# Optimization experiments

Hardware: AMD Instinct MI355X
Metric: run time of the kernel (lower is better)

Reference implementation:

```python
import jax, jax.numpy as jnp
from jax import lax
import numpy as np

NUM_HEAD = 4
D_MODEL = 160
HEAD_DIM = D_MODEL // NUM_HEAD  # 40
FEAT_DIM = 64
F_SIZE = (128, 128)
B = 4
LN_EPS = 1e-5
LEAKY_SLOPE = 0.01
DN = ('NCHW', 'OIHW', 'NCHW')


def setup_inputs() -> dict:
    key = jax.random.key(0)
    ks = jax.random.split(key, 10)
    pe_len = (F_SIZE[0] // 2) * (F_SIZE[1] // 2) + 1  # 4097
    s = 0.05
    return {
        'x': jax.random.normal(ks[0], (B, FEAT_DIM, F_SIZE[0], F_SIZE[1]), jnp.float32),
        'conv1_w': jax.random.normal(ks[1], (FEAT_DIM, FEAT_DIM, 2, 2), jnp.float32) * s,
        'conv1_b': jax.random.normal(ks[2], (FEAT_DIM,), jnp.float32) * s,
        'conv2_w': jax.random.normal(ks[3], (D_MODEL, FEAT_DIM, 1, 1), jnp.float32) * s,
        'conv2_b': jax.random.normal(ks[4], (D_MODEL,), jnp.float32) * s,
        'pe': jax.random.uniform(ks[5], (pe_len, 1), jnp.float32),
        'wq': jax.random.normal(ks[6], (D_MODEL, D_MODEL), jnp.float32) * s,
        'wk': jax.random.normal(ks[7], (D_MODEL, D_MODEL), jnp.float32) * s,
        'wv': jax.random.normal(ks[8], (D_MODEL, D_MODEL), jnp.float32) * s,
        'ln_w': jnp.ones((D_MODEL,), jnp.float32),
        'ln_b': jnp.zeros((D_MODEL,), jnp.float32),
    }


def reference(x, conv1_w, conv1_b, conv2_w, conv2_b, pe, wq, wk, wv, ln_w, ln_b):
    b = x.shape[0]
    # patch embed: stride-2 conv -> 1x1 conv -> LeakyReLU
    f = lax.conv_general_dilated(x, conv1_w, (2, 2), 'VALID', dimension_numbers=DN)
    f = f + conv1_b[None, :, None, None]
    f = lax.conv_general_dilated(f, conv2_w, (1, 1), 'VALID', dimension_numbers=DN)
    f = f + conv2_b[None, :, None, None]
    f = jnp.where(f >= 0, f, LEAKY_SLOPE * f)
    _, c, h, w = f.shape  # [b, 160, 64, 64]
    f = f.reshape(b, c, h * w).transpose(0, 2, 1)  # [b, s, d]
    # pad one extra token at end of sequence, add positional encoding [s+1, 1]
    f = jnp.pad(f, ((0, 0), (0, 1), (0, 0))) + pe  # [b, s+1, d]
    s1 = f.shape[1]
    # torch Linear (no bias): y = x @ W.T
    q = (f @ wq.T).reshape(b, s1, NUM_HEAD, HEAD_DIM).transpose(0, 2, 1, 3)
    k = (f @ wk.T).reshape(b, s1, NUM_HEAD, HEAD_DIM).transpose(0, 2, 1, 3)
    v = (f @ wv.T).reshape(b, s1, NUM_HEAD, HEAD_DIM).transpose(0, 2, 1, 3)
    score = jnp.einsum('bhqd,bhkd->bhqk', q, k) / jnp.sqrt(jnp.float32(HEAD_DIM))
    score = jax.nn.softmax(score, axis=-1)
    att = jnp.einsum('bhqk,bhkd->bhqd', score, v)  # [b, h, s+1, hd]
    cat = att.transpose(0, 2, 1, 3).reshape(b, s1, D_MODEL)
    feat = cat[:, :-1, :]  # drop padded token -> [b, s, d]
    # residual LayerNorm: LN(feat) + feat
    mu = jnp.mean(feat, axis=-1, keepdims=True)
    var = jnp.mean(jnp.square(feat - mu), axis=-1, keepdims=True)
    ln = (feat - mu) / jnp.sqrt(var + LN_EPS) * ln_w + ln_b
    feat = ln + feat
    feat = feat.transpose(0, 2, 1).reshape(b, D_MODEL, h, w)  # [b, 160, 64, 64]
    feat = jnp.repeat(jnp.repeat(feat, 2, axis=2), 2, axis=3)
    return feat
```

## Files before the change

### kernel.cpp

```cpp
#include <hip/hip_runtime.h>

typedef _Float16 f16;
typedef _Float16 half2v __attribute__((ext_vector_type(2)));
typedef _Float16 half4v __attribute__((ext_vector_type(4)));
typedef _Float16 half8 __attribute__((ext_vector_type(8)));
typedef float f32x4 __attribute__((ext_vector_type(4)));
typedef unsigned u32x4 __attribute__((ext_vector_type(4)));

#define MFMA16(a, b, c) __builtin_amdgcn_mfma_f32_16x16x32_f16((a), (b), (c), 0, 0, 0)

__device__ __forceinline__ unsigned pk2(float a, float b) {
  return __builtin_bit_cast(unsigned, __builtin_amdgcn_cvt_pkrtz(a, b));
}

__device__ __forceinline__ void plswap_pair(unsigned& a, unsigned& b) {
  asm("s_nop 1\n\t"
      "v_permlane32_swap_b32 %0, %1\n\t"
      "v_permlane16_swap_b32 %0, %1"
      : "+v"(a), "+v"(b));
}


__global__ __launch_bounds__(256) void k_convqkv(
    const float* __restrict__ x, const float* __restrict__ w1, const float* __restrict__ b1,
    const float* __restrict__ w2, const float* __restrict__ b2, const float* __restrict__ pe,
    const float* __restrict__ wq, const float* __restrict__ wk, const float* __restrict__ wv,
    f16* __restrict__ q_h, f16* __restrict__ k_h, f16* __restrict__ vt_h,
    float* __restrict__ kmaxp) {
  __shared__ __attribute__((aligned(16))) char smem[112192];
  f16* fT   = (f16*)smem;
  f16* xh   = (f16*)(smem + 21504);
  f16* wT   = (f16*)(smem + 21504);
  float* red = (float*)(smem + 48384);
  f16* w1h  = (f16*)(smem + 55360);
  f16* c1t  = (f16*)(smem + 55360);
  f16* Lv   = (f16*)(smem + 55360);
  float* red160 = (float*)(smem + 64576);
  f16* w2h  = (f16*)(smem + 89152);

  const float c1l = 0.15811388300841898f * 1.4426950408889634f;

  int y = blockIdx.x, b = blockIdx.y;
  int t = threadIdx.x, lane = t & 63, wv4 = t >> 6, quad = lane >> 4, col = lane & 15;
  int s0 = y * 64;

  const float* xb = x + (b * 64) * 16384 + (2 * y) * 128;
#pragma unroll
  for (int it = 0; it < 32; ++it) {
    int flat = t + it * 256;
    int pos = flat & 63, r = (flat >> 6) & 1, ci = flat >> 7;
    float2 v = *(const float2*)(xb + ci * 16384 + r * 128 + 2 * pos);
    *(unsigned*)(xh + pos * 264 + ci * 4 + r * 2) = pk2(v.x, v.y);
  }
#pragma unroll
  for (int it = 0; it < 16; ++it) {
    int i4 = t + it * 256;
    int co = i4 >> 6, q4 = (i4 & 63) * 4;
    f32x4 v = *(const f32x4*)(w1 + co * 256 + q4);
    uint2 u = {pk2(v[0], v[1]), pk2(v[2], v[3])};
    *(uint2*)(w1h + co * 264 + q4) = u;
  }
#pragma unroll
  for (int it = 0; it < 10; ++it) {
    int i4 = t + it * 256;
    int c2 = i4 >> 4, q4 = (i4 & 15) * 4;
    f32x4 v = *(const f32x4*)(w2 + c2 * 64 + q4);
    uint2 u = {pk2(v[0], v[1]), pk2(v[2], v[3])};
    *(uint2*)(w2h + c2 * 72 + q4) = u;
  }
  __syncthreads();

  float b1v[4];
#pragma unroll
  for (int r = 0; r < 4; ++r) b1v[r] = b1[wv4 * 16 + quad * 4 + r];
  f32x4 acc1[4];
#pragma unroll
  for (int nt = 0; nt < 4; ++nt)
#pragma unroll
    for (int r = 0; r < 4; ++r) acc1[nt][r] = b1v[r];
#pragma unroll
  for (int kk = 0; kk < 8; ++kk) {
    half8 a = *(half8*)(w1h + (wv4 * 16 + col) * 264 + kk * 32 + quad * 8);
#pragma unroll
    for (int nt = 0; nt < 4; ++nt) {
      half8 bfr = *(half8*)(xh + (nt * 16 + col) * 264 + kk * 32 + quad * 8);
      acc1[nt] = MFMA16(a, bfr, acc1[nt]);
    }
  }
  __syncthreads();
#pragma unroll
  for (int nt = 0; nt < 4; ++nt) {
    uint2 u = {pk2(acc1[nt][0], acc1[nt][1]), pk2(acc1[nt][2], acc1[nt][3])};
    *(uint2*)(c1t + (nt * 16 + col) * 72 + wv4 * 16 + quad * 4) = u;
  }
  __syncthreads();

  f32x4 acc2[10];
#pragma unroll
  for (int mt = 0; mt < 10; ++mt)
#pragma unroll
    for (int r = 0; r < 4; ++r) acc2[mt][r] = b2[mt * 16 + quad * 4 + r];
  half8 bb0 = *(half8*)(c1t + (wv4 * 16 + col) * 72 + quad * 8);
  half8 bb1 = *(half8*)(c1t + (wv4 * 16 + col) * 72 + 32 + quad * 8);
#pragma unroll
  for (int mt = 0; mt < 10; ++mt) {
    half8 a0 = *(half8*)(w2h + (mt * 16 + col) * 72 + quad * 8);
    half8 a1 = *(half8*)(w2h + (mt * 16 + col) * 72 + 32 + quad * 8);
    acc2[mt] = MFMA16(a0, bb0, acc2[mt]);
    acc2[mt] = MFMA16(a1, bb1, acc2[mt]);
  }
  float pes = pe[s0 + wv4 * 16 + col];
#pragma unroll
  for (int mt = 0; mt < 10; ++mt) {
    float p[4];
#pragma unroll
    for (int r = 0; r < 4; ++r) {
      float v = acc2[mt][r];
      v = (v >= 0.f) ? v : 0.01f * v;
      p[r] = v + pes;
    }
    uint2 u = {pk2(p[0], p[1]), pk2(p[2], p[3])};
    *(uint2*)(fT + (wv4 * 16 + col) * 168 + mt * 16 + quad * 4) = u;
  }
  __syncthreads();

  half8 af[5];
  int rowA = wv4 * 16 + col;
#pragma unroll
  for (int kk = 0; kk < 5; ++kk)
    af[kk] = *(half8*)(fT + rowA * 168 + kk * 32 + quad * 8);

  float ks0[4], ks1[4];
#pragma unroll
  for (int r = 0; r < 4; ++r) { ks0[r] = 0.f; ks1[r] = 0.f; }

  for (int kind = 0; kind < 3; ++kind) {
    const float* wsp = (kind == 0) ? wq : (kind == 1 ? wk : wv);
    for (int hf = 0; hf < 2; ++hf) {
      __syncthreads();
      for (int c = t; c < 1600; c += 256) {
        int row = c / 20, seg = c - row * 20;
        const float* src = wsp + (hf * 80 + row) * 160 + seg * 8;
        f32x4 va = *(const f32x4*)src;
        f32x4 vb = *(const f32x4*)(src + 4);
        uint4 u = {pk2(va[0], va[1]), pk2(va[2], va[3]), pk2(vb[0], vb[1]), pk2(vb[2], vb[3])};
        *(uint4*)(wT + row * 168 + seg * 8) = u;
      }
      __syncthreads();
#pragma unroll
      for (int n0 = 0; n0 < 5; ++n0) {
        f32x4 acc; acc[0] = 0.f; acc[1] = 0.f; acc[2] = 0.f; acc[3] = 0.f;
        int rowB = n0 * 16 + col;
#pragma unroll
        for (int kk = 0; kk < 5; ++kk) {
          half8 bf = *(half8*)(wT + rowB * 168 + kk * 32 + quad * 8);
          acc = MFMA16(af[kk], bf, acc);
        }
        int o = (hf * 5 + n0) * 16 + col;
        int hh = o / 40, d = o - hh * 40;
        int bh = b * 4 + hh;
        if (kind == 1) {
          bool kidx = (n0 * 16 + col) >= 40;
#pragma unroll
          for (int r = 0; r < 4; ++r) {
            float z = acc[r] * acc[r];
            ks0[r] += kidx ? 0.f : z;
            ks1[r] += kidx ? z : 0.f;
          }
        }
        if (kind == 2) {
          half4v hv;
#pragma unroll
          for (int r = 0; r < 4; ++r) hv[r] = (f16)acc[r];
          *(half4v*)(Lv + (n0 * 16 + col) * 72 + wv4 * 16 + quad * 4) = hv;
        } else {
#pragma unroll
          for (int r = 0; r < 4; ++r) {
            int s = s0 + wv4 * 16 + quad * 4 + r;
            if (kind == 0)      q_h[((size_t)bh * 4097 + s) * 40 + d] = (f16)(acc[r] * c1l);
            else                k_h[((size_t)bh * 4160 + s) * 40 + d] = (f16)acc[r];
          }
        }
      }
      if (kind == 1) {
        float m0 = 0.f, m1 = 0.f;
#pragma unroll
        for (int r = 0; r < 4; ++r) {
          float v0 = ks0[r], v1 = ks1[r];
          v0 += __shfl_xor(v0, 1); v0 += __shfl_xor(v0, 2);
          v0 += __shfl_xor(v0, 4); v0 += __shfl_xor(v0, 8);
          v1 += __shfl_xor(v1, 1); v1 += __shfl_xor(v1, 2);
          v1 += __shfl_xor(v1, 4); v1 += __shfl_xor(v1, 8);
          m0 = fmaxf(m0, v0); m1 = fmaxf(m1, v1);
          ks0[r] = 0.f; ks1[r] = 0.f;
        }
        m0 = fmaxf(m0, __shfl_xor(m0, 16)); m0 = fmaxf(m0, __shfl_xor(m0, 32));
        m1 = fmaxf(m1, __shfl_xor(m1, 16)); m1 = fmaxf(m1, __shfl_xor(m1, 32));
        if (lane == 0) { red[wv4 * 4 + hf * 2] = m0; red[wv4 * 4 + hf * 2 + 1] = m1; }
      }
      if (kind == 2) {
        __syncthreads();
        for (int c = t; c < 640; c += 256) {
          int row = c >> 3, seg = c & 7;
          int o = hf * 80 + row, hh = o / 40, d = o - hh * 40;
          *(uint4*)(vt_h + ((size_t)(b * 4 + hh) * 40 + d) * 4160 + s0 + seg * 8) =
              *(const uint4*)(Lv + row * 72 + seg * 8);
        }
      }
    }
  }
  __syncthreads();
  if (t < 4) {
    float m = fmaxf(fmaxf(red[t], red[4 + t]), fmaxf(red[8 + t], red[12 + t]));
    kmaxp[(b * 4 + t) * 65 + y] = m;
  }

  if (y == 63) {
    float pe4 = pe[4096];
    if (t < 160) {
      int hh = t / 40, d = t - hh * 40, bh = b * 4 + hh;
#pragma unroll
      for (int kind = 0; kind < 3; ++kind) {
        const float* wsp = (kind == 0) ? wq : (kind == 1 ? wk : wv);
        const float* wr = wsp + t * 160;
        float rs = 0.f;
#pragma unroll
        for (int c4 = 0; c4 < 40; ++c4) {
          f32x4 v = *(const f32x4*)(wr + c4 * 4);
          rs += v[0] + v[1] + v[2] + v[3];
        }
        float val = pe4 * rs;
        if (kind == 0)      q_h[((size_t)bh * 4097 + 4096) * 40 + d] = (f16)(val * c1l);
        else if (kind == 1) { k_h[((size_t)bh * 4160 + 4096) * 40 + d] = (f16)val;
                              red160[t] = val * val; }
        else                vt_h[((size_t)bh * 40 + d) * 4160 + 4096] = (f16)val;
      }
    }
    __syncthreads();
    if (t < 4) {
      float s = 0.f;
#pragma unroll
      for (int j = 0; j < 40; ++j) s += red160[t * 40 + j];
      kmaxp[(b * 4 + t) * 65 + 64] = s;
    }
  }
}

__global__ __launch_bounds__(256, 6) void k_attn(
    const f16* __restrict__ q_h, const f16* __restrict__ k_h,
    const f16* __restrict__ vt_h, const float* __restrict__ kmaxp,
    float* __restrict__ pacc) {
  __shared__ __attribute__((aligned(16))) f16 Ks[2][64 * 40];
  __shared__ __attribute__((aligned(16))) f16 Vs[2][40 * 72];
  __shared__ __attribute__((aligned(16))) f16 Ones[8];
  __shared__ __attribute__((aligned(16))) f16 Zro[8];
  __shared__ __attribute__((aligned(16))) float red4[4];

  int qt = blockIdx.x, bh = blockIdx.y, ks = blockIdx.z;
  int qbase = qt * 128;
  int t = threadIdx.x, lane = t & 63, wv = t >> 6, quad = lane >> 4, col = lane & 15;
  int gbase = ks * 22;
  int nIter = (ks == 2) ? 21 : 22;

  if (t < 8) { Zro[t] = (f16)0; Ones[t] = (f16)1; }
  {
    float vm = (t < 65) ? kmaxp[bh * 65 + t] : 0.f;
#pragma unroll
    for (int d = 1; d < 64; d <<= 1) vm = fmaxf(vm, __shfl_xor(vm, d));
    if (lane == 0) red4[wv] = vm;
  }

  const f16* khb = k_h + ((size_t)bh * 4160 + gbase * 64) * 40;
  const f16* vtb = vt_h + (size_t)bh * 40 * 4160;
  int vrow = t >> 3, vseg = t & 7;
  uint4 rka = *(const uint4*)(khb + t * 8);
  uint4 rkb = {0, 0, 0, 0}, rvb = {0, 0, 0, 0};
  if (t < 64) rkb = *(const uint4*)(khb + (256 + t) * 8);
  uint4 rva = *(const uint4*)(vtb + vrow * 4160 + gbase * 64 + vseg * 8);
  if (t < 64) rvb = *(const uint4*)(vtb + (32 + vrow) * 4160 + gbase * 64 + vseg * 8);

  half8 zero8;
#pragma unroll
  for (int j = 0; j < 8; ++j) zero8[j] = (f16)0;

  half8 bq[2][2], q32[2];
#pragma unroll
  for (int nt = 0; nt < 2; ++nt) {
    const f16* qr = q_h + ((size_t)bh * 4097 + qbase + wv * 32 + nt * 16 + col) * 40;
    bq[nt][0] = *(const half8*)(qr + quad * 8);
    q32[nt] = *(const half8*)(qr + 32);
  }
  __syncthreads();

  float mk = fmaxf(fmaxf(red4[0], red4[1]), fmaxf(red4[2], red4[3]));

#pragma unroll
  for (int nt = 0; nt < 2; ++nt) {
    float s = 0.f;
#pragma unroll
    for (int j = 0; j < 8; ++j) {
      float a0 = (float)bq[nt][0][j];
      s += a0 * a0;
    }
    s += __shfl_xor(s, 16);
    s += __shfl_xor(s, 32);
#pragma unroll
    for (int j = 0; j < 8; ++j) {
      float a1 = (float)q32[nt][j];
      s += a1 * a1;
    }
    float mfl = sqrtf(s * mk) - 14.0f;
    half8 e = zero8;
    e[0] = (f16)(-mfl);
    bq[nt][1] = (quad == 0) ? q32[nt] : ((quad == 1) ? e : zero8);
  }

  f32x4 o_[2][3];
#pragma unroll
  for (int a = 0; a < 2; ++a)
#pragma unroll
    for (int b2 = 0; b2 < 3; ++b2)
#pragma unroll
      for (int r = 0; r < 4; ++r) o_[a][b2][r] = 0.f;

  for (int kt = 0; kt < nIter; ++kt) {
    int bsel = kt & 1;
    int g = gbase + kt;
    *(uint4*)(&Ks[bsel][t * 8]) = rka;
    if (t < 64) *(uint4*)(&Ks[bsel][(256 + t) * 8]) = rkb;
    *(uint4*)(&Vs[bsel][vrow * 72 + vseg * 8]) = rva;
    if (t < 64) *(uint4*)(&Vs[bsel][(32 + vrow) * 72 + vseg * 8]) = rvb;
    if (kt + 1 < nIter) {
      const f16* kn = khb + (size_t)(kt + 1) * 2560;
      int k0n = (g + 1) << 6;
      rka = *(const uint4*)(kn + t * 8);
      if (t < 64) rkb = *(const uint4*)(kn + (256 + t) * 8);
      rva = *(const uint4*)(vtb + vrow * 4160 + k0n + vseg * 8);
      if (t < 64) rvb = *(const uint4*)(vtb + (32 + vrow) * 4160 + k0n + vseg * 8);
    }
    __syncthreads();

    bool lastt = (g == 64);
#pragma unroll
    for (int kk2 = 0; kk2 < 2; ++kk2) {
      f32x4 acc[2][2];
#pragma unroll
      for (int hf = 0; hf < 2; ++hf) {
        int mt = kk2 * 2 + hf;
        int row = mt * 16 + col;
        half8 ak0 = *(half8*)(&Ks[bsel][row * 40 + quad * 8]);
        const f16* pa1 = (quad == 0) ? &Ks[bsel][row * 40 + 32]
                                     : ((quad == 1) ? Ones : Zro);
        half8 ak1 = *(half8*)pa1;
#pragma unroll
        for (int nt = 0; nt < 2; ++nt) {
          f32x4 a; a[0] = 0.f; a[1] = 0.f; a[2] = 0.f; a[3] = 0.f;
          a = MFMA16(ak0, bq[nt][0], a);
          a = MFMA16(ak1, bq[nt][1], a);
          acc[hf][nt] = a;
        }
      }
      half8 pa[2];
#pragma unroll
      for (int nt = 0; nt < 2; ++nt) {
        float p0[4], p1[4];
#pragma unroll
        for (int r = 0; r < 4; ++r) {
          p0[r] = __builtin_amdgcn_exp2f(acc[0][nt][r]);
          p1[r] = __builtin_amdgcn_exp2f(acc[1][nt][r]);
        }
        if (__builtin_expect(lastt, 0)) {
#pragma unroll
          for (int r = 0; r < 4; ++r) {
            p0[r] = ((kk2 * 2) * 16 + quad * 4 + r) == 0 ? p0[r] : 0.f;
            p1[r] = 0.f;
          }
        }
        unsigned sr[4];
        sr[0] = pk2(p0[0], p0[1]);
        sr[1] = pk2(p0[2], p0[3]);
        sr[2] = pk2(p1[0], p1[1]);
        sr[3] = pk2(p1[2], p1[3]);
        plswap_pair(sr[0], sr[2]);
        plswap_pair(sr[1], sr[3]);
        u32x4 uu; uu[0] = sr[0]; uu[1] = sr[1]; uu[2] = sr[2]; uu[3] = sr[3];
        pa[nt] = __builtin_bit_cast(half8, uu);
      }
#pragma unroll
      for (int nv = 0; nv < 3; ++nv) {
        int d = nv * 16 + col;
        const f16* vp = (d < 40) ? &Vs[bsel][d * 72 + kk2 * 32 + quad * 8]
                                 : ((d == 40) ? Ones : Zro);
        half8 bv = *(half8*)vp;
        o_[0][nv] = MFMA16(pa[0], bv, o_[0][nv]);
        o_[1][nv] = MFMA16(pa[1], bv, o_[1][nv]);
      }
    }
  }

  float* pb = pacc + (size_t)(ks * 16 + bh) * 4096 * 48;
#pragma unroll
  for (int mtq = 0; mtq < 2; ++mtq)
#pragma unroll
    for (int nv = 0; nv < 3; ++nv)
#pragma unroll
      for (int r = 0; r < 4; ++r) {
        int q = qbase + wv * 32 + mtq * 16 + quad * 4 + r;
        pb[(size_t)q * 48 + nv * 16 + col] = o_[mtq][nv][r];
      }
}

__global__ __launch_bounds__(256) void k_ln_out(
    const float* __restrict__ pacc, const float* __restrict__ lnw,
    const float* __restrict__ lnb, float* __restrict__ out) {
  __shared__ float g[32 * 164];
  __shared__ float linv[32 * 4];
  int y = blockIdx.x, b = blockIdx.y, z = blockIdx.z, t = threadIdx.x;
  const size_t P1 = (size_t)16 * 4096 * 48;
  int w0 = z * 32;
  if (t < 128) {
    int row = t >> 2, h = t & 3;
    size_t i0 = ((size_t)(b * 4 + h) * 4096 + y * 64 + w0 + row) * 48 + 40;
    linv[row * 4 + h] = 1.f / (pacc[i0] + pacc[P1 + i0] + pacc[2 * P1 + i0]);
  }
  __syncthreads();
#pragma unroll
  for (int it = 0; it < 5; ++it) {
    int flat = t + it * 256;
    int row = flat / 40, dq = flat - row * 40;
    int h = dq / 10, d = (dq - h * 10) * 4;
    size_t idx = ((size_t)(b * 4 + h) * 4096 + y * 64 + w0 + row) * 48 + d;
    f32x4 v0 = *(const f32x4*)(pacc + idx);
    f32x4 v1 = *(const f32x4*)(pacc + P1 + idx);
    f32x4 v2 = *(const f32x4*)(pacc + 2 * P1 + idx);
    float li = linv[row * 4 + h];
    f32x4 gv;
#pragma unroll
    for (int j = 0; j < 4; ++j) gv[j] = (v0[j] + v1[j] + v2[j]) * li;
    *(f32x4*)(g + row * 164 + h * 40 + d) = gv;
  }
  __syncthreads();
  int row = t >> 3, part = t & 7;
  float* gr = g + row * 164 + part * 20;
  float s1 = 0.f, s2 = 0.f;
#pragma unroll
  for (int j4 = 0; j4 < 5; ++j4) {
    f32x4 v = *(f32x4*)(gr + j4 * 4);
#pragma unroll
    for (int j = 0; j < 4; ++j) { s1 += v[j]; s2 += v[j] * v[j]; }
  }
  s1 += __shfl_xor(s1, 1); s1 += __shfl_xor(s1, 2); s1 += __shfl_xor(s1, 4);
  s2 += __shfl_xor(s2, 1); s2 += __shfl_xor(s2, 2); s2 += __shfl_xor(s2, 4);
  float mu = s1 * (1.f / 160.f);
  float var = s2 * (1.f / 160.f) - mu * mu;
  float inv = rsqrtf(var + 1e-5f);
  const float* lw = lnw + part * 20;
  const float* lb = lnb + part * 20;
#pragma unroll
  for (int j = 0; j < 20; ++j) {
    float v = gr[j];
    gr[j] = (v - mu) * inv * lw[j] + lb[j] + v;
  }
  __syncthreads();
  int Yo = t >> 7, xp = t & 63, cpar = (t >> 6) & 1;
  int rl = xp >> 1;
  float* ob = out + (2 * y + Yo) * 128 + z * 64 + xp;
  for (int c = cpar; c < 160; c += 2)
    ob[(size_t)(b * 160 + c) * 16384] = g[rl * 164 + c];
}

extern "C" void kernel_launch(void* const* d_in, const int* in_sizes, int n_in,
                              void* d_out, int out_size, void* d_ws, size_t ws_size,
                              hipStream_t stream) {
  const float* x   = (const float*)d_in[0];
  const float* w1  = (const float*)d_in[1];
  const float* b1  = (const float*)d_in[2];
  const float* w2  = (const float*)d_in[3];
  const float* b2  = (const float*)d_in[4];
  const float* pe  = (const float*)d_in[5];
  const float* wq  = (const float*)d_in[6];
  const float* wk  = (const float*)d_in[7];
  const float* wvp = (const float*)d_in[8];
  const float* lnw = (const float*)d_in[9];
  const float* lnb = (const float*)d_in[10];
  float* out = (float*)d_out;

  char* p = (char*)d_ws;
  f16* q_h   = (f16*)p;   p += (size_t)16 * 4097 * 40 * 2;
  f16* k_h   = (f16*)p;   p += (size_t)16 * 4160 * 40 * 2;
  f16* vt_h  = (f16*)p;   p += (size_t)16 * 40 * 4160 * 2;
  float* pacc = (float*)p; p += (size_t)3 * 16 * 4096 * 48 * 4;
  float* kmaxp = (float*)p; p += 16 * 65 * 4;

  k_convqkv<<<dim3(64, 4), 256, 0, stream>>>(x, w1, b1, w2, b2, pe, wq, wk, wvp,
                                             q_h, k_h, vt_h, kmaxp);
  k_attn<<<dim3(32, 16, 3), 256, 0, stream>>>(q_h, k_h, vt_h, kmaxp, pacc);
  k_ln_out<<<dim3(64, 4, 2), 256, 0, stream>>>(pacc, lnw, lnb, out);
}
```

Before: 245.9 us.

## Split attention keys into two chunks and batch QK MFMAs per tile

The key-sequence split in the attention kernel drops from three partitions to two (33 and 32 tiles). The partial-accumulator buffer and the LayerNorm combine step shrink to match, so one partial buffer is no longer written and read. Each 64-key tile now computes all four QK score blocks before the exp and PV stage, which gives more independent MFMAs per tile but uses more registers, so the occupancy hint drops from 6 to 4 blocks. This cuts partial-result traffic, but the grid falls to 1024 blocks and per-block serial work grows.

```diff
diff --git a/kernel.cpp b/kernel.cpp
--- a/kernel.cpp
+++ b/kernel.cpp
@@ -246,7 +246,7 @@
   }
 }
 
-__global__ __launch_bounds__(256, 6) void k_attn(
+__global__ __launch_bounds__(256, 4) void k_attn(
     const f16* __restrict__ q_h, const f16* __restrict__ k_h,
     const f16* __restrict__ vt_h, const float* __restrict__ kmaxp,
     float* __restrict__ pacc) {
@@ -259,8 +259,8 @@
   int qt = blockIdx.x, bh = blockIdx.y, ks = blockIdx.z;
   int qbase = qt * 128;
   int t = threadIdx.x, lane = t & 63, wv = t >> 6, quad = lane >> 4, col = lane & 15;
-  int gbase = ks * 22;
-  int nIter = (ks == 2) ? 21 : 22;
+  int gbase = ks * 33;
+  int nIter = 33 - ks;
 
   if (t < 8) { Zro[t] = (f16)0; Ones[t] = (f16)1; }
   {
@@ -341,38 +341,39 @@
     __syncthreads();
 
     bool lastt = (g == 64);
-#pragma unroll
-    for (int kk2 = 0; kk2 < 2; ++kk2) {
-      f32x4 acc[2][2];
-#pragma unroll
-      for (int hf = 0; hf < 2; ++hf) {
-        int mt = kk2 * 2 + hf;
-        int row = mt * 16 + col;
-        half8 ak0 = *(half8*)(&Ks[bsel][row * 40 + quad * 8]);
-        const f16* pa1 = (quad == 0) ? &Ks[bsel][row * 40 + 32]
-                                     : ((quad == 1) ? Ones : Zro);
-        half8 ak1 = *(half8*)pa1;
-#pragma unroll
-        for (int nt = 0; nt < 2; ++nt) {
-          f32x4 a; a[0] = 0.f; a[1] = 0.f; a[2] = 0.f; a[3] = 0.f;
-          a = MFMA16(ak0, bq[nt][0], a);
-          a = MFMA16(ak1, bq[nt][1], a);
-          acc[hf][nt] = a;
-        }
-      }
-      half8 pa[2];
+
+    f32x4 acc[4][2];
+#pragma unroll
+    for (int mt = 0; mt < 4; ++mt) {
+      int row = mt * 16 + col;
+      half8 ak0 = *(half8*)(&Ks[bsel][row * 40 + quad * 8]);
+      const f16* pa1 = (quad == 0) ? &Ks[bsel][row * 40 + 32]
+                                   : ((quad == 1) ? Ones : Zro);
+      half8 ak1 = *(half8*)pa1;
+#pragma unroll
+      for (int nt = 0; nt < 2; ++nt) {
+        f32x4 a; a[0] = 0.f; a[1] = 0.f; a[2] = 0.f; a[3] = 0.f;
+        a = MFMA16(ak0, bq[nt][0], a);
+        a = MFMA16(ak1, bq[nt][1], a);
+        acc[mt][nt] = a;
+      }
+    }
+
+    half8 pa[2][2];
+#pragma unroll
+    for (int kk2 = 0; kk2 < 2; ++kk2)
 #pragma unroll
       for (int nt = 0; nt < 2; ++nt) {
         float p0[4], p1[4];
 #pragma unroll
         for (int r = 0; r < 4; ++r) {
-          p0[r] = __builtin_amdgcn_exp2f(acc[0][nt][r]);
-          p1[r] = __builtin_amdgcn_exp2f(acc[1][nt][r]);
+          p0[r] = __builtin_amdgcn_exp2f(acc[kk2 * 2][nt][r]);
+          p1[r] = __builtin_amdgcn_exp2f(acc[kk2 * 2 + 1][nt][r]);
         }
         if (__builtin_expect(lastt, 0)) {
 #pragma unroll
           for (int r = 0; r < 4; ++r) {
-            p0[r] = ((kk2 * 2) * 16 + quad * 4 + r) == 0 ? p0[r] : 0.f;
+            p0[r] = (kk2 == 0 && (quad * 4 + r) == 0) ? p0[r] : 0.f;
             p1[r] = 0.f;
           }
         }
@@ -384,18 +385,20 @@
         plswap_pair(sr[0], sr[2]);
         plswap_pair(sr[1], sr[3]);
         u32x4 uu; uu[0] = sr[0]; uu[1] = sr[1]; uu[2] = sr[2]; uu[3] = sr[3];
-        pa[nt] = __builtin_bit_cast(half8, uu);
-      }
+        pa[kk2][nt] = __builtin_bit_cast(half8, uu);
+      }
+
+#pragma unroll
+    for (int kk2 = 0; kk2 < 2; ++kk2)
 #pragma unroll
       for (int nv = 0; nv < 3; ++nv) {
         int d = nv * 16 + col;
         const f16* vp = (d < 40) ? &Vs[bsel][d * 72 + kk2 * 32 + quad * 8]
                                  : ((d == 40) ? Ones : Zro);
         half8 bv = *(half8*)vp;
-        o_[0][nv] = MFMA16(pa[0], bv, o_[0][nv]);
-        o_[1][nv] = MFMA16(pa[1], bv, o_[1][nv]);
-      }
-    }
+        o_[0][nv] = MFMA16(pa[kk2][0], bv, o_[0][nv]);
+        o_[1][nv] = MFMA16(pa[kk2][1], bv, o_[1][nv]);
+      }
   }
 
   float* pb = pacc + (size_t)(ks * 16 + bh) * 4096 * 48;
@@ -421,7 +424,7 @@
   if (t < 128) {
     int row = t >> 2, h = t & 3;
     size_t i0 = ((size_t)(b * 4 + h) * 4096 + y * 64 + w0 + row) * 48 + 40;
-    linv[row * 4 + h] = 1.f / (pacc[i0] + pacc[P1 + i0] + pacc[2 * P1 + i0]);
+    linv[row * 4 + h] = 1.f / (pacc[i0] + pacc[P1 + i0]);
   }
   __syncthreads();
 #pragma unroll
@@ -432,11 +435,10 @@
     size_t idx = ((size_t)(b * 4 + h) * 4096 + y * 64 + w0 + row) * 48 + d;
     f32x4 v0 = *(const f32x4*)(pacc + idx);
     f32x4 v1 = *(const f32x4*)(pacc + P1 + idx);
-    f32x4 v2 = *(const f32x4*)(pacc + 2 * P1 + idx);
     float li = linv[row * 4 + h];
     f32x4 gv;
 #pragma unroll
-    for (int j = 0; j < 4; ++j) gv[j] = (v0[j] + v1[j] + v2[j]) * li;
+    for (int j = 0; j < 4; ++j) gv[j] = (v0[j] + v1[j]) * li;
     *(f32x4*)(g + row * 164 + h * 40 + d) = gv;
   }
   __syncthreads();
@@ -489,11 +491,11 @@
   f16* q_h   = (f16*)p;   p += (size_t)16 * 4097 * 40 * 2;
   f16* k_h   = (f16*)p;   p += (size_t)16 * 4160 * 40 * 2;
   f16* vt_h  = (f16*)p;   p += (size_t)16 * 40 * 4160 * 2;
-  float* pacc = (float*)p; p += (size_t)3 * 16 * 4096 * 48 * 4;
+  float* pacc = (float*)p; p += (size_t)2 * 16 * 4096 * 48 * 4;
   float* kmaxp = (float*)p; p += 16 * 65 * 4;
 
   k_convqkv<<<dim3(64, 4), 256, 0, stream>>>(x, w1, b1, w2, b2, pe, wq, wk, wvp,
                                              q_h, k_h, vt_h, kmaxp);
-  k_attn<<<dim3(32, 16, 3), 256, 0, stream>>>(q_h, k_h, vt_h, kmaxp, pacc);
+  k_attn<<<dim3(32, 16, 2), 256, 0, stream>>>(q_h, k_h, vt_h, kmaxp, pacc);
   k_ln_out<<<dim3(64, 4, 2), 256, 0, stream>>>(pacc, lnw, lnb, out);
 }
```

Measured after the change: 201.2 us. 18.2% less time.
